# Kernel tuning notes

Measured on AMD Instinct MI355X. Metric: run time of the kernel, lower is better.

The kernel has to match this reference:

```python
import jax, jax.numpy as jnp
import numpy as np

N_NODES = 8192
N_EDGES = 262144  # avg degree 32
F_IN = 128
F_OUT = 128


def setup_inputs() -> dict:
    key = jax.random.key(0)
    k1, k2, k3, k4 = jax.random.split(key, 4)
    x = jax.random.normal(k1, (N_NODES, F_IN), dtype=jnp.float32)
    edge_index = jax.random.randint(k2, (2, N_EDGES), 0, N_NODES, dtype=jnp.int32)
    # xavier_uniform-scale random W; B is a learned param (zeros at init, but
    # use random values so the x@B^T branch is exercised numerically)
    scale = np.float32(1.0 / np.sqrt(F_IN))
    W = jax.random.normal(k3, (F_OUT, F_IN), dtype=jnp.float32) * scale
    B = jax.random.normal(k4, (F_OUT, F_IN), dtype=jnp.float32) * scale
    return {"x": x, "edge_index": edge_index, "W": W, "B": B}


def reference(x, edge_index, W, B):
    num_nodes = x.shape[0]
    src, dst = edge_index[0], edge_index[1]
    # Dense adjacency: A[i, j] = 1 iff edge j -> i (duplicate edges collapse to 1,
    # matching torch's adj[dst, src] = 1.0 assignment semantics)
    A = jnp.zeros((num_nodes, num_nodes), dtype=jnp.float32).at[dst, src].set(1.0)
    # In-degree (counts duplicate edges, matching torch.bincount); degree-0 -> 1
    deg = jax.ops.segment_sum(jnp.ones_like(dst, dtype=jnp.float32), dst,
                              num_segments=num_nodes)
    deg = jnp.where(deg == 0, 1.0, deg)
    # D_inv @ A @ x @ W^T + x @ B^T; D_inv is diagonal -> row-scale by 1/deg
    msg = A @ (x @ W.T)           # [N, F_OUT]
    out = msg / deg[:, None] + x @ B.T
    return out
```

## Files before the change

### kernel.cpp

```cpp
#include <hip/hip_runtime.h>
#include <hip/hip_bf16.h>

constexpr int NN = 8192;
constexpr int NE = 262144;
constexpr int FD = 128;
constexpr int CAP = 64;

constexpr size_t H_OFF     = 0;
constexpr size_t H_BYTES   = (size_t)NN * FD * 2;
constexpr size_t CNT_OFF   = H_OFF + H_BYTES;
constexpr size_t CNT_BYTES = (size_t)NN * 4;
constexpr size_t COL_OFF   = CNT_OFF + CNT_BYTES;
constexpr size_t COL_BYTES = (size_t)NN * CAP * 4;
constexpr size_t UB_OFF    = COL_OFF + COL_BYTES;

constexpr int FILL_BLOCKS = 512;
constexpr int GEMM_BLOCKS = 256;

typedef __attribute__((ext_vector_type(8))) short short8;
typedef __attribute__((ext_vector_type(4))) float f32x4;

__device__ __forceinline__ short f2b(float f) {
  union { __hip_bfloat16 b; short s; } u;
  u.b = __float2bfloat16(f);
  return u.s;
}

__global__ __launch_bounds__(256) void prep_kernel(
    const float* __restrict__ W, const float* __restrict__ Bm,
    short* __restrict__ ub, unsigned int* __restrict__ cnt) {
  const int t = blockIdx.x * 256 + threadIdx.x;
  const float4 f = (t < 4096) ? ((const float4*)W)[t] : ((const float4*)Bm)[t - 4096];
  ((short4*)ub)[t] = short4{f2b(f.x), f2b(f.y), f2b(f.z), f2b(f.w)};
  if (t < 2048) ((uint4*)cnt)[t] = uint4{0u, 0u, 0u, 0u};
}

__global__ __launch_bounds__(256) void fillgemm_kernel(
    const int* __restrict__ ei, unsigned int* __restrict__ cnt,
    int* __restrict__ col, const float* __restrict__ x,
    const short* __restrict__ ub, __hip_bfloat16* __restrict__ h,
    float* __restrict__ out) {
  const int tid = threadIdx.x;

  if (blockIdx.x < FILL_BLOCKS) {
    const int e = (blockIdx.x * 256 + tid) * 2;
    const int2 s2 = *(const int2*)(ei + e);
    const int2 d2 = *(const int2*)(ei + NE + e);
#pragma unroll
    for (int r = 0; r < 2; ++r) {
      const int src = (&s2.x)[r];
      const int dst = (&d2.x)[r];
      const unsigned int pos = atomicAdd(&cnt[dst], 1u);
      if (pos < CAP) col[(size_t)dst * CAP + pos] = src;
    }
    return;
  }

  const int gid = blockIdx.x - FILL_BLOCKS;
  const int bm = (gid >> 2) * 128;
  const int bn = (gid & 3) * 64;
  const int w = tid >> 6;
  const int lane = tid & 63;
  const int l15 = lane & 15;
  const int l4 = lane >> 4;
  const int row0 = bm + w * 32;

  f32x4 acc[2][4] = {};

#pragma unroll
  for (int kk = 0; kk < 4; ++kk) {
    const int koff = kk * 32 + l4 * 8;
    const float4* xp0 = (const float4*)(x + (size_t)(row0 + l15) * FD + koff);
    const float4* xp1 = (const float4*)(x + (size_t)(row0 + 16 + l15) * FD + koff);
    const float4 p0 = xp0[0], p1 = xp0[1];
    const float4 q0 = xp1[0], q1 = xp1[1];
    const short8 a0 = short8{f2b(p0.x), f2b(p0.y), f2b(p0.z), f2b(p0.w),
                             f2b(p1.x), f2b(p1.y), f2b(p1.z), f2b(p1.w)};
    const short8 a1 = short8{f2b(q0.x), f2b(q0.y), f2b(q0.z), f2b(q0.w),
                             f2b(q1.x), f2b(q1.y), f2b(q1.z), f2b(q1.w)};
#pragma unroll
    for (int ni = 0; ni < 4; ++ni) {
      const short8 b = *(const short8*)(ub + (size_t)(bn + ni * 16 + l15) * FD + koff);
      acc[0][ni] = __builtin_amdgcn_mfma_f32_16x16x32_bf16(a0, b, acc[0][ni], 0, 0, 0);
      acc[1][ni] = __builtin_amdgcn_mfma_f32_16x16x32_bf16(a1, b, acc[1][ni], 0, 0, 0);
    }
  }

#pragma unroll
  for (int mi = 0; mi < 2; ++mi) {
#pragma unroll
    for (int ni = 0; ni < 4; ++ni) {
      const int n = bn + ni * 16 + l15;
#pragma unroll
      for (int r = 0; r < 4; ++r) {
        const int row = row0 + mi * 16 + l4 * 4 + r;
        const float v = acc[mi][ni][r];
        if (n < FD) h[(size_t)row * FD + n] = __float2bfloat16(v);
        else        out[(size_t)row * FD + (n - FD)] = v;
      }
    }
  }
}

__global__ __launch_bounds__(256) void gather_kernel(
    const unsigned int* __restrict__ h,
    const int* __restrict__ col, const unsigned int* __restrict__ cnt,
    float* __restrict__ out) {
  __shared__ unsigned int bmp[4][NN / 32];

  const int w    = threadIdx.x >> 6;
  const int lane = threadIdx.x & 63;
  const int node = blockIdx.x * 4 + w;
  const int c  = lane & 15;
  const int eu = lane >> 4;
  const unsigned int n = cnt[node];
  const unsigned int nn = (n < (unsigned)CAP) ? n : (unsigned)CAP;
  const int* cl = col + (size_t)node * CAP;

  const int colv = cl[lane];

  ((uint4*)bmp[w])[lane] = uint4{0u, 0u, 0u, 0u};
  __syncthreads();

  int keep = colv;
  if (lane < (int)nn) {
    const unsigned int mask = 1u << (colv & 31);
    const unsigned int old = atomicOr(&bmp[w][colv >> 5], mask);
    if (old & mask) keep = -1;
  }

  float acc[8];
#pragma unroll
  for (int i = 0; i < 8; ++i) acc[i] = 0.f;

  const size_t hstride = FD / 2;

  unsigned int base = 0;
  for (; base + 8 <= nn; base += 8) {
    const int s0 = __shfl(keep, (int)(base + eu), 64);
    const int s1 = __shfl(keep, (int)(base + 4 + eu), 64);
    uint4 v0 = uint4{0u,0u,0u,0u}, v1 = uint4{0u,0u,0u,0u};
    if (s0 >= 0) v0 = *(const uint4*)(h + (size_t)s0 * hstride + (c << 2));
    if (s1 >= 0) v1 = *(const uint4*)(h + (size_t)s1 * hstride + (c << 2));
    acc[0] += __uint_as_float(v0.x << 16) + __uint_as_float(v1.x << 16);
    acc[1] += __uint_as_float(v0.x & 0xffff0000u) + __uint_as_float(v1.x & 0xffff0000u);
    acc[2] += __uint_as_float(v0.y << 16) + __uint_as_float(v1.y << 16);
    acc[3] += __uint_as_float(v0.y & 0xffff0000u) + __uint_as_float(v1.y & 0xffff0000u);
    acc[4] += __uint_as_float(v0.z << 16) + __uint_as_float(v1.z << 16);
    acc[5] += __uint_as_float(v0.z & 0xffff0000u) + __uint_as_float(v1.z & 0xffff0000u);
    acc[6] += __uint_as_float(v0.w << 16) + __uint_as_float(v1.w << 16);
    acc[7] += __uint_as_float(v0.w & 0xffff0000u) + __uint_as_float(v1.w & 0xffff0000u);
  }
  if (base < nn) {
    const unsigned int e0 = base + eu;
    const unsigned int e1 = base + 4 + eu;
    const int s0 = __shfl(keep, (int)e0, 64);
    const int s1 = __shfl(keep, (int)e1, 64);
    uint4 v0 = uint4{0u,0u,0u,0u}, v1 = uint4{0u,0u,0u,0u};
    if (e0 < nn && s0 >= 0) v0 = *(const uint4*)(h + (size_t)s0 * hstride + (c << 2));
    if (e1 < nn && s1 >= 0) v1 = *(const uint4*)(h + (size_t)s1 * hstride + (c << 2));
    acc[0] += __uint_as_float(v0.x << 16) + __uint_as_float(v1.x << 16);
    acc[1] += __uint_as_float(v0.x & 0xffff0000u) + __uint_as_float(v1.x & 0xffff0000u);
    acc[2] += __uint_as_float(v0.y << 16) + __uint_as_float(v1.y << 16);
    acc[3] += __uint_as_float(v0.y & 0xffff0000u) + __uint_as_float(v1.y & 0xffff0000u);
    acc[4] += __uint_as_float(v0.z << 16) + __uint_as_float(v1.z << 16);
    acc[5] += __uint_as_float(v0.z & 0xffff0000u) + __uint_as_float(v1.z & 0xffff0000u);
    acc[6] += __uint_as_float(v0.w << 16) + __uint_as_float(v1.w << 16);
    acc[7] += __uint_as_float(v0.w & 0xffff0000u) + __uint_as_float(v1.w & 0xffff0000u);
  }

#pragma unroll
  for (int i = 0; i < 8; ++i) {
    acc[i] += __shfl_xor(acc[i], 16, 64);
    acc[i] += __shfl_xor(acc[i], 32, 64);
  }

  if (eu == 0) {
    const float r = 1.0f / (n ? (float)n : 1.0f);
    float* op = out + (size_t)node * FD + c * 8;
    float4 o0 = *(float4*)op;
    float4 o1 = *(float4*)(op + 4);
    o0.x += acc[0] * r; o0.y += acc[1] * r; o0.z += acc[2] * r; o0.w += acc[3] * r;
    o1.x += acc[4] * r; o1.y += acc[5] * r; o1.z += acc[6] * r; o1.w += acc[7] * r;
    *(float4*)op = o0;
    *(float4*)(op + 4) = o1;
  }
}

extern "C" void kernel_launch(void* const* d_in, const int* in_sizes, int n_in,
                              void* d_out, int out_size, void* d_ws, size_t ws_size,
                              hipStream_t stream) {
  const float* x  = (const float*)d_in[0];
  const int* ei   = (const int*)d_in[1];
  const float* W  = (const float*)d_in[2];
  const float* Bm = (const float*)d_in[3];
  float* out = (float*)d_out;

  char* ws = (char*)d_ws;
  __hip_bfloat16* h = (__hip_bfloat16*)(ws + H_OFF);
  unsigned int* cnt = (unsigned int*)(ws + CNT_OFF);
  int* col          = (int*)(ws + COL_OFF);
  short* ub         = (short*)(ws + UB_OFF);

  prep_kernel<<<32, 256, 0, stream>>>(W, Bm, ub, cnt);
  fillgemm_kernel<<<FILL_BLOCKS + GEMM_BLOCKS, 256, 0, stream>>>(
      ei, cnt, col, x, ub, h, out);
  gather_kernel<<<NN / 4, 256, 0, stream>>>((const unsigned int*)h, col, cnt, out);
}
```

Baseline: 36.21 us.

## Fold prep kernel into fused fill/GEMM kernel with flag-based intra-grid sync

```diff
diff --git a/kernel.cpp b/kernel.cpp
--- a/kernel.cpp
+++ b/kernel.cpp
@@ -12,10 +12,14 @@
 constexpr size_t CNT_BYTES = (size_t)NN * 4;
 constexpr size_t COL_OFF   = CNT_OFF + CNT_BYTES;
 constexpr size_t COL_BYTES = (size_t)NN * CAP * 4;
-constexpr size_t UB_OFF    = COL_OFF + COL_BYTES;
-
+constexpr size_t FLAG_OFF  = COL_OFF + COL_BYTES;
+
+constexpr unsigned int MAGIC = 0x5CA1AB1Eu;
+
+constexpr int GEMM_BLOCKS = 256;
 constexpr int FILL_BLOCKS = 512;
-constexpr int GEMM_BLOCKS = 256;
+constexpr int FILL_FIRST  = 1 + GEMM_BLOCKS;
+constexpr int FUSED_BLOCKS = FILL_FIRST + FILL_BLOCKS;
 
 typedef __attribute__((ext_vector_type(8))) short short8;
 typedef __attribute__((ext_vector_type(4))) float f32x4;
@@ -26,24 +30,40 @@
   return u.s;
 }
 
-__global__ __launch_bounds__(256) void prep_kernel(
-    const float* __restrict__ W, const float* __restrict__ Bm,
-    short* __restrict__ ub, unsigned int* __restrict__ cnt) {
-  const int t = blockIdx.x * 256 + threadIdx.x;
-  const float4 f = (t < 4096) ? ((const float4*)W)[t] : ((const float4*)Bm)[t - 4096];
-  ((short4*)ub)[t] = short4{f2b(f.x), f2b(f.y), f2b(f.z), f2b(f.w)};
-  if (t < 2048) ((uint4*)cnt)[t] = uint4{0u, 0u, 0u, 0u};
-}
-
-__global__ __launch_bounds__(256) void fillgemm_kernel(
+__device__ __forceinline__ short8 cvt8(float4 a, float4 b) {
+  return short8{f2b(a.x), f2b(a.y), f2b(a.z), f2b(a.w),
+                f2b(b.x), f2b(b.y), f2b(b.z), f2b(b.w)};
+}
+
+__global__ __launch_bounds__(256) void fused_kernel(
     const int* __restrict__ ei, unsigned int* __restrict__ cnt,
     int* __restrict__ col, const float* __restrict__ x,
-    const short* __restrict__ ub, __hip_bfloat16* __restrict__ h,
-    float* __restrict__ out) {
+    const float* __restrict__ W, const float* __restrict__ Bm,
+    __hip_bfloat16* __restrict__ h, float* __restrict__ out,
+    unsigned int* __restrict__ flag) {
   const int tid = threadIdx.x;
-
-  if (blockIdx.x < FILL_BLOCKS) {
-    const int e = (blockIdx.x * 256 + tid) * 2;
+  const int bid = blockIdx.x;
+
+  if (bid == 0) {
+    uint4* c4 = (uint4*)cnt;
+#pragma unroll
+    for (int i = 0; i < 8; ++i) c4[tid + i * 256] = uint4{0u, 0u, 0u, 0u};
+    __syncthreads();
+    __threadfence();
+    if (tid == 0)
+      __hip_atomic_store(flag, MAGIC, __ATOMIC_RELEASE, __HIP_MEMORY_SCOPE_AGENT);
+    return;
+  }
+
+  if (bid >= FILL_FIRST) {
+    if (tid == 0) {
+      while (__hip_atomic_load(flag, __ATOMIC_ACQUIRE, __HIP_MEMORY_SCOPE_AGENT)
+             != MAGIC)
+        __builtin_amdgcn_s_sleep(8);
+    }
+    __syncthreads();
+
+    const int e = ((bid - FILL_FIRST) * 256 + tid) * 2;
     const int2 s2 = *(const int2*)(ei + e);
     const int2 d2 = *(const int2*)(ei + NE + e);
 #pragma unroll
@@ -56,7 +76,7 @@
     return;
   }
 
-  const int gid = blockIdx.x - FILL_BLOCKS;
+  const int gid = bid - 1;
   const int bm = (gid >> 2) * 128;
   const int bn = (gid & 3) * 64;
   const int w = tid >> 6;
@@ -65,6 +85,9 @@
   const int l4 = lane >> 4;
   const int row0 = bm + w * 32;
 
+  const float* Usrc = (bn < FD) ? W : Bm;
+  const int ubase = bn & (FD - 1);
+
   f32x4 acc[2][4] = {};
 
 #pragma unroll
@@ -72,15 +95,12 @@
     const int koff = kk * 32 + l4 * 8;
     const float4* xp0 = (const float4*)(x + (size_t)(row0 + l15) * FD + koff);
     const float4* xp1 = (const float4*)(x + (size_t)(row0 + 16 + l15) * FD + koff);
-    const float4 p0 = xp0[0], p1 = xp0[1];
-    const float4 q0 = xp1[0], q1 = xp1[1];
-    const short8 a0 = short8{f2b(p0.x), f2b(p0.y), f2b(p0.z), f2b(p0.w),
-                             f2b(p1.x), f2b(p1.y), f2b(p1.z), f2b(p1.w)};
-    const short8 a1 = short8{f2b(q0.x), f2b(q0.y), f2b(q0.z), f2b(q0.w),
-                             f2b(q1.x), f2b(q1.y), f2b(q1.z), f2b(q1.w)};
+    const short8 a0 = cvt8(xp0[0], xp0[1]);
+    const short8 a1 = cvt8(xp1[0], xp1[1]);
 #pragma unroll
     for (int ni = 0; ni < 4; ++ni) {
-      const short8 b = *(const short8*)(ub + (size_t)(bn + ni * 16 + l15) * FD + koff);
+      const float4* up = (const float4*)(Usrc + (size_t)(ubase + ni * 16 + l15) * FD + koff);
+      const short8 b = cvt8(up[0], up[1]);
       acc[0][ni] = __builtin_amdgcn_mfma_f32_16x16x32_bf16(a0, b, acc[0][ni], 0, 0, 0);
       acc[1][ni] = __builtin_amdgcn_mfma_f32_16x16x32_bf16(a1, b, acc[1][ni], 0, 0, 0);
     }
@@ -105,7 +125,10 @@
 __global__ __launch_bounds__(256) void gather_kernel(
     const unsigned int* __restrict__ h,
     const int* __restrict__ col, const unsigned int* __restrict__ cnt,
-    float* __restrict__ out) {
+    float* __restrict__ out, unsigned int* __restrict__ flag) {
+  if (blockIdx.x == 0 && threadIdx.x == 0)
+    __hip_atomic_store(flag, 0u, __ATOMIC_RELAXED, __HIP_MEMORY_SCOPE_AGENT);
+
   __shared__ unsigned int bmp[4][NN / 32];
 
   const int w    = threadIdx.x >> 6;
@@ -197,13 +220,11 @@
   float* out = (float*)d_out;
 
   char* ws = (char*)d_ws;
-  __hip_bfloat16* h = (__hip_bfloat16*)(ws + H_OFF);
-  unsigned int* cnt = (unsigned int*)(ws + CNT_OFF);
-  int* col          = (int*)(ws + COL_OFF);
-  short* ub         = (short*)(ws + UB_OFF);
-
-  prep_kernel<<<32, 256, 0, stream>>>(W, Bm, ub, cnt);
-  fillgemm_kernel<<<FILL_BLOCKS + GEMM_BLOCKS, 256, 0, stream>>>(
-      ei, cnt, col, x, ub, h, out);
-  gather_kernel<<<NN / 4, 256, 0, stream>>>((const unsigned int*)h, col, cnt, out);
-}
+  __hip_bfloat16* h  = (__hip_bfloat16*)(ws + H_OFF);
+  unsigned int* cnt  = (unsigned int*)(ws + CNT_OFF);
+  int* col           = (int*)(ws + COL_OFF);
+  unsigned int* flag = (unsigned int*)(ws + FLAG_OFF);
+
+  fused_kernel<<<FUSED_BLOCKS, 256, 0, stream>>>(ei, cnt, col, x, W, Bm, h, out, flag);
+  gather_kernel<<<NN / 4, 256, 0, stream>>>((const unsigned int*)h, col, cnt, out, flag);
+}
```

Result: slower. 46.42 us (+28.2%).
